# Kernel optimization log

Hardware: AMD Instinct MI355X
Metric: run time of the kernel (lower is better)

The kernel has to match this reference:

```python
import jax, jax.numpy as jnp
import numpy as np

B, T, D, C = 8, 4096, 768, 2048

def setup_inputs() -> dict:
    key = jax.random.key(0)
    k1, k2 = jax.random.split(key)
    embed = jax.random.normal(k1, (B, T, D), dtype=jnp.float32)
    cluster_centers = jax.random.normal(k2, (C, D), dtype=jnp.float32)
    return {"embed": embed, "cluster_centers": cluster_centers}

def reference(embed, cluster_centers):
    x_sq = jnp.sum(embed * embed, axis=-1, keepdims=True)          # (b, t, 1)
    c_sq = jnp.sum(cluster_centers * cluster_centers, axis=-1)     # (c,)
    cross = jnp.einsum('btd,cd->btc', embed, cluster_centers)      # (b, t, c)
    sq_dists = x_sq + c_sq[None, None, :] - 2.0 * cross
    dists = jnp.sqrt(jnp.maximum(sq_dists, 0.0))
    # dists argmax of -cdist == argmin of cdist
    clusters = jnp.argmin(dists, axis=-1)                          # (b, t) int
    return clusters
```

## Files before the change

kernel.cpp:

```cpp
#include <hip/hip_runtime.h>

typedef __fp16 f16x2 __attribute__((ext_vector_type(2)));
typedef __fp16 f16x8 __attribute__((ext_vector_type(8)));
typedef float f32x4 __attribute__((ext_vector_type(4)));

constexpr int MM = 32768;
constexpr int NN = 2048;
constexpr int KK = 768;
constexpr int NKT = KK / 32;
constexpr int NA_UNITS = (MM / 16) * NKT;
constexpr int NB_UNITS = (NN / 16) * NKT;

constexpr size_t WS_APACK = 0;
constexpr size_t WS_BPACK = WS_APACK + (size_t)MM * KK * 4;
constexpr size_t WS_CSQ   = WS_BPACK + (size_t)NN * KK * 4;
constexpr size_t WS_SLOT  = WS_CSQ + (size_t)NN * 4;
constexpr size_t WS_NEED  = WS_SLOT + (size_t)MM * 16 * 8;

__device__ __forceinline__ unsigned bc(f16x2 h) {
    return __builtin_bit_cast(unsigned, h);
}


__global__ __launch_bounds__(256)
void fragpack_kernel(const float* __restrict__ A, const float* __restrict__ Bc,
                     uint4* __restrict__ Ap, uint4* __restrict__ Bp,
                     float* __restrict__ csq) {
    const int task = blockIdx.x * 4 + (threadIdx.x >> 6);
    const int lane = threadIdx.x & 63;

    if (task >= NA_UNITS + NB_UNITS) {
        const int cl = task - (NA_UNITS + NB_UNITS);
        const float4* row = reinterpret_cast<const float4*>(Bc + (size_t)cl * KK);
        float s = 0.f;
#pragma unroll
        for (int w = 0; w < KK / (4 * 64); ++w) {
            float4 v = row[w * 64 + lane];
            s = fmaf(v.x, v.x, s); s = fmaf(v.y, v.y, s);
            s = fmaf(v.z, v.z, s); s = fmaf(v.w, v.w, s);
        }
#pragma unroll
        for (int off = 32; off > 0; off >>= 1) s += __shfl_xor(s, off, 64);
        if (lane == 0) csq[cl] = s;
        return;
    }

    const int ln15 = lane & 15;
    const int quad = lane >> 4;

    const bool isB = task >= NA_UNITS;
    const int t = isB ? task - NA_UNITS : task;
    const int tile = t / NKT, kt = t % NKT;
    const float* src = (isB ? Bc : A) + (size_t)(tile * 16 + ln15) * KK + kt * 32 + quad * 8;
    uint4* dst = (isB ? Bp : Ap) + (size_t)t * 128 + lane;

    const float4 v0 = *(const float4*)(src);
    const float4 v1 = *(const float4*)(src + 4);
    f16x2 h0 = __builtin_amdgcn_cvt_pkrtz(v0.x, v0.y);
    f16x2 h1 = __builtin_amdgcn_cvt_pkrtz(v0.z, v0.w);
    f16x2 h2 = __builtin_amdgcn_cvt_pkrtz(v1.x, v1.y);
    f16x2 h3 = __builtin_amdgcn_cvt_pkrtz(v1.z, v1.w);
    f16x2 l0 = __builtin_amdgcn_cvt_pkrtz(v0.x-(float)h0[0], v0.y-(float)h0[1]);
    f16x2 l1 = __builtin_amdgcn_cvt_pkrtz(v0.z-(float)h1[0], v0.w-(float)h1[1]);
    f16x2 l2 = __builtin_amdgcn_cvt_pkrtz(v1.x-(float)h2[0], v1.y-(float)h2[1]);
    f16x2 l3 = __builtin_amdgcn_cvt_pkrtz(v1.z-(float)h3[0], v1.w-(float)h3[1]);
    uint4 hv = {bc(h0), bc(h1), bc(h2), bc(h3)};
    uint4 lv = {bc(l0), bc(l1), bc(l2), bc(l3)};
    dst[0]  = hv;
    dst[64] = lv;
}

__global__ __launch_bounds__(64)
void csq_kernel(const float* __restrict__ cc, float* __restrict__ csq) {
    const int cl = blockIdx.x;
    const int lane = threadIdx.x;
    const float4* row = reinterpret_cast<const float4*>(cc + (size_t)cl * KK);
    float s = 0.f;
#pragma unroll
    for (int w = 0; w < KK / (4 * 64); ++w) {
        float4 v = row[w * 64 + lane];
        s = fmaf(v.x, v.x, s); s = fmaf(v.y, v.y, s);
        s = fmaf(v.z, v.z, s); s = fmaf(v.w, v.w, s);
    }
#pragma unroll
    for (int off = 32; off > 0; off >>= 1) s += __shfl_xor(s, off, 64);
    if (lane == 0) csq[cl] = s;
}

#define MF2(a, b, c) __builtin_amdgcn_mfma_f32_16x16x32_f16(a, b, c, 0, 0, 0)
#define DSB() __builtin_amdgcn_sched_barrier(0)

__global__ __launch_bounds__(256, 2)
void gemm_pack_kernel(const uint4* __restrict__ Ap, const uint4* __restrict__ Bp,
                      const float* __restrict__ csq, uint2* __restrict__ slots) {
    __shared__ uint4 ldsq[4096];

    const int b   = blockIdx.x;
    const int xcd = b & 7;
    const int s   = b >> 3;
    const int gx  = s & 15;
    const int gy  = xcd + ((s >> 4) << 3);

    const int tid  = threadIdx.x;
    const int lane = tid & 63;
    const int ln15 = lane & 15;
    const int quad = lane >> 4;
    const int wave = tid >> 6;
    const int wm   = wave >> 1;
    const int wn   = wave & 1;
    const int tbase = gy * 128;
    const int cb    = gx * 128;

    const uint4* sp[8];
#pragma unroll
    for (int q = 0; q < 8; ++q) {
        const int u = wave * 8 + q;
        const bool isA = u < 16;
        const int v = isA ? u : u - 16;
        const int tile = (isA ? gy * 8 : gx * 8) + (v >> 1);
        const int part = v & 1;
        sp[q] = (isA ? Ap : Bp) + (size_t)tile * NKT * 128 + part * 64 + lane;
    }

#define STAGE2(kt_, bufq_, q_) {                                              \
    _Pragma("unroll")                                                         \
    for (int qq = (q_); qq < (q_) + 2; ++qq)                                  \
        __builtin_amdgcn_global_load_lds(                                     \
            (const __attribute__((address_space(1))) unsigned int*)(sp[qq] + (kt_) * 128), \
            (__attribute__((address_space(3))) unsigned int*)&ldsq[(bufq_) + (wave * 8 + qq) * 64], \
            16, 0, 0); }

    f32x4 acc[4][4];
#pragma unroll
    for (int i = 0; i < 4; ++i)
#pragma unroll
        for (int j = 0; j < 4; ++j) { f32x4 z = {0.f,0.f,0.f,0.f}; acc[i][j] = z; }

    f16x8 Bh[4], Bl[4];
    f16x8 Ah[2], Al[2];

#define RD_B(bufq_) {                                                         \
    _Pragma("unroll")                                                         \
    for (int j = 0; j < 4; ++j) {                                             \
        const int nu = 16 + (wn * 4 + j) * 2;                                 \
        Bh[j] = *(const f16x8*)&ldsq[(bufq_) + nu * 64 + lane];               \
        Bl[j] = *(const f16x8*)&ldsq[(bufq_) + (nu + 1) * 64 + lane];         \
    } }

#define RD_A(bufq_, i_, s_) {                                                 \
    const int au = (wm * 4 + (i_)) * 2;                                       \
    Ah[s_] = *(const f16x8*)&ldsq[(bufq_) + au * 64 + lane];                  \
    Al[s_] = *(const f16x8*)&ldsq[(bufq_) + (au + 1) * 64 + lane]; }

#define MFMA_I(i_, s_) {                                                      \
    __builtin_amdgcn_s_setprio(1);                                            \
    _Pragma("unroll")                                                         \
    for (int j = 0; j < 4; ++j) acc[i_][j] = MF2(Ah[s_], Bh[j], acc[i_][j]);  \
    _Pragma("unroll")                                                         \
    for (int j = 0; j < 4; ++j) acc[i_][j] = MF2(Ah[s_], Bl[j], acc[i_][j]);  \
    _Pragma("unroll")                                                         \
    for (int j = 0; j < 4; ++j) acc[i_][j] = MF2(Al[s_], Bh[j], acc[i_][j]);  \
    __builtin_amdgcn_s_setprio(0); }

    STAGE2(0, 0, 0) STAGE2(0, 0, 2) STAGE2(0, 0, 4) STAGE2(0, 0, 6)

#pragma unroll 1
    for (int kt = 0; kt < NKT; ++kt) {
        const int bufq = (kt & 1) ? 2048 : 0;
        const int nxt  = bufq ^ 2048;
        const bool sn  = (kt + 1 < NKT);

        if (sn) {
            STAGE2(kt + 1, nxt, 0)
            asm volatile("s_waitcnt vmcnt(2)" ::: "memory");
        } else {
            asm volatile("s_waitcnt vmcnt(0)" ::: "memory");
        }
        DSB(); __builtin_amdgcn_s_barrier(); DSB();

        RD_B(bufq)
        RD_A(bufq, 0, 0)
        DSB();
        RD_A(bufq, 1, 1)
        if (sn) STAGE2(kt + 1, nxt, 2)
        DSB();
        MFMA_I(0, 0)
        DSB();
        RD_A(bufq, 2, 0)
        if (sn) STAGE2(kt + 1, nxt, 4)
        DSB();
        MFMA_I(1, 1)
        DSB();
        RD_A(bufq, 3, 1)
        if (sn) STAGE2(kt + 1, nxt, 6)
        DSB();
        MFMA_I(2, 0)
        DSB();
        MFMA_I(3, 1)
        DSB(); __builtin_amdgcn_s_barrier(); DSB();
    }

    float csq4[4];
#pragma unroll
    for (int j = 0; j < 4; ++j) csq4[j] = csq[cb + wn * 64 + j * 16 + ln15];

    float bval[16]; int bidx[16];
#pragma unroll
    for (int i = 0; i < 4; ++i)
#pragma unroll
        for (int r = 0; r < 4; ++r) {
            const int rid = i * 4 + r;
            float bv_ = csq4[0] - 2.0f * acc[i][0][r];
            int   bi_ = cb + wn * 64 + ln15;
#pragma unroll
            for (int j = 1; j < 4; ++j) {
                const float s2 = csq4[j] - 2.0f * acc[i][j][r];
                const int   c = cb + wn * 64 + j * 16 + ln15;
                if (s2 < bv_) { bv_ = s2; bi_ = c; }
            }
            bval[rid] = bv_; bidx[rid] = bi_;
        }
#pragma unroll
    for (int off = 1; off < 16; off <<= 1) {
#pragma unroll
        for (int rid = 0; rid < 16; ++rid) {
            const float ov = __shfl_xor(bval[rid], off, 64);
            const int   oi = __shfl_xor(bidx[rid], off, 64);
            if (ov < bval[rid] || (ov == bval[rid] && oi < bidx[rid])) {
                bval[rid] = ov; bidx[rid] = oi;
            }
        }
    }

    __syncthreads();
    float* vtab = (float*)&ldsq[0];
    int*   itab = (int*)&ldsq[64];
    if (ln15 == 0) {
#pragma unroll
        for (int i = 0; i < 4; ++i)
#pragma unroll
            for (int r = 0; r < 4; ++r) {
                const int row = wm * 64 + i * 16 + quad * 4 + r;
                vtab[row * 2 + wn] = bval[i * 4 + r];
                itab[row * 2 + wn] = bidx[i * 4 + r];
            }
    }
    __syncthreads();
    if (tid < 128) {
        float v0 = vtab[tid * 2]; int i0 = itab[tid * 2];
        const float v1 = vtab[tid * 2 + 1]; const int i1 = itab[tid * 2 + 1];
        if (v1 < v0 || (v1 == v0 && i1 < i0)) { v0 = v1; i0 = i1; }
        uint2 e; e.x = __float_as_uint(v0); e.y = (unsigned)i0;
        slots[(size_t)(tbase + tid) * 16 + gx] = e;
    }
}

__global__ __launch_bounds__(256)
void slot_reduce_kernel(const uint2* __restrict__ slots, int* __restrict__ out) {
    const int t = blockIdx.x * 256 + threadIdx.x;
    const uint2* s = slots + (size_t)t * 16;
    float bv = __uint_as_float(s[0].x); int bi = (int)s[0].y;
#pragma unroll
    for (int j = 1; j < 16; ++j) {
        const uint2 e = s[j];
        const float v = __uint_as_float(e.x);
        if (v < bv || (v == bv && (int)e.y < bi)) { bv = v; bi = (int)e.y; }
    }
    out[t] = bi;
}


__global__ __launch_bounds__(256)
void init_ws_kernel(unsigned long long* __restrict__ w) {
    w[blockIdx.x * 256 + threadIdx.x] = 0xFFFFFFFFFFFFFFFFull;
}

__global__ __launch_bounds__(256, 2)
void argmin_mfma_kernel(const float* __restrict__ A, const float* __restrict__ Bc,
                        const float* __restrict__ csq,
                        unsigned long long* __restrict__ ws64) {
    __shared__ unsigned lds[4 * 128 * 20];
    constexpr int AH = 0, AL = 2560, BH = 5120;

    const int tid  = threadIdx.x;
    const int lane = tid & 63;
    const int ln15 = lane & 15;
    const int quad = lane >> 4;
    const int wave = tid >> 6;
    const int wm = wave >> 1, wn = wave & 1;
    const int tbase = blockIdx.x * 128;
    const int cb    = blockIdx.y * 128;

    const int sr  = tid >> 1;
    const int skh = tid & 1;
    const float* gA = A  + (size_t)(tbase + sr) * KK + skh * 16;
    const float* gB = Bc + (size_t)(cb   + sr) * KK + skh * 16;
    const int wword = sr * 20 + skh * 8;

    f32x4 acc[4][4];
#pragma unroll
    for (int i = 0; i < 4; ++i)
#pragma unroll
        for (int j = 0; j < 4; ++j) { f32x4 z = {0.f,0.f,0.f,0.f}; acc[i][j] = z; }

    float4 av[4], bv[4];
#pragma unroll
    for (int p = 0; p < 4; ++p) {
        av[p] = *(const float4*)(gA + p * 4);
        bv[p] = *(const float4*)(gB + p * 4);
    }

    int aw[4], bw[4];
#pragma unroll
    for (int i = 0; i < 4; ++i) {
        aw[i] = AH + (wm * 64 + i * 16 + ln15) * 20 + quad * 4;
        bw[i] = BH + (wn * 64 + i * 16 + ln15) * 20 + quad * 4;
    }

    for (int k0 = 0; k0 < KK; k0 += 32) {
        __syncthreads();
#pragma unroll
        for (int h = 0; h < 2; ++h) {
            float4 v0 = av[2*h], v1 = av[2*h+1];
            f16x2 h00 = __builtin_amdgcn_cvt_pkrtz(v0.x, v0.y);
            f16x2 h01 = __builtin_amdgcn_cvt_pkrtz(v0.z, v0.w);
            f16x2 h10 = __builtin_amdgcn_cvt_pkrtz(v1.x, v1.y);
            f16x2 h11 = __builtin_amdgcn_cvt_pkrtz(v1.z, v1.w);
            f16x2 l00 = __builtin_amdgcn_cvt_pkrtz(v0.x-(float)h00[0], v0.y-(float)h00[1]);
            f16x2 l01 = __builtin_amdgcn_cvt_pkrtz(v0.z-(float)h01[0], v0.w-(float)h01[1]);
            f16x2 l10 = __builtin_amdgcn_cvt_pkrtz(v1.x-(float)h10[0], v1.y-(float)h10[1]);
            f16x2 l11 = __builtin_amdgcn_cvt_pkrtz(v1.z-(float)h11[0], v1.w-(float)h11[1]);
            uint4 hv = {bc(h00), bc(h01), bc(h10), bc(h11)};
            uint4 lv = {bc(l00), bc(l01), bc(l10), bc(l11)};
            *(uint4*)&lds[AH + wword + 4*h] = hv;
            *(uint4*)&lds[AL + wword + 4*h] = lv;

            float4 w0 = bv[2*h], w1 = bv[2*h+1];
            f16x2 g00 = __builtin_amdgcn_cvt_pkrtz(w0.x, w0.y);
            f16x2 g01 = __builtin_amdgcn_cvt_pkrtz(w0.z, w0.w);
            f16x2 g10 = __builtin_amdgcn_cvt_pkrtz(w1.x, w1.y);
            f16x2 g11 = __builtin_amdgcn_cvt_pkrtz(w1.z, w1.w);
            f16x2 m00 = __builtin_amdgcn_cvt_pkrtz(w0.x-(float)g00[0], w0.y-(float)g00[1]);
            f16x2 m01 = __builtin_amdgcn_cvt_pkrtz(w0.z-(float)g01[0], w0.w-(float)g01[1]);
            f16x2 m10 = __builtin_amdgcn_cvt_pkrtz(w1.x-(float)g10[0], w1.y-(float)g10[1]);
            f16x2 m11 = __builtin_amdgcn_cvt_pkrtz(w1.z-(float)g11[0], w1.w-(float)g11[1]);
            uint4 gv = {bc(g00), bc(g01), bc(g10), bc(g11)};
            uint4 mv = {bc(m00), bc(m01), bc(m10), bc(m11)};
            *(uint4*)&lds[BH + wword + 4*h]        = gv;
            *(uint4*)&lds[BH + 2560 + wword + 4*h] = mv;
        }
        __syncthreads();

        const int kn = k0 + 32;
        if (kn < KK) {
#pragma unroll
            for (int p = 0; p < 4; ++p) {
                av[p] = *(const float4*)(gA + kn + p * 4);
                bv[p] = *(const float4*)(gB + kn + p * 4);
            }
        }

        f16x8 a_h[4], a_l[4], b_h[4], b_l[4];
#pragma unroll
        for (int i = 0; i < 4; ++i) {
            a_h[i] = *(const f16x8*)&lds[aw[i]];
            a_l[i] = *(const f16x8*)&lds[aw[i] + 2560];
            b_h[i] = *(const f16x8*)&lds[bw[i]];
            b_l[i] = *(const f16x8*)&lds[bw[i] + 2560];
        }
#pragma unroll
        for (int i = 0; i < 4; ++i)
#pragma unroll
            for (int j = 0; j < 4; ++j) {
                acc[i][j] = __builtin_amdgcn_mfma_f32_16x16x32_f16(a_h[i], b_h[j], acc[i][j], 0, 0, 0);
                acc[i][j] = __builtin_amdgcn_mfma_f32_16x16x32_f16(a_h[i], b_l[j], acc[i][j], 0, 0, 0);
                acc[i][j] = __builtin_amdgcn_mfma_f32_16x16x32_f16(a_l[i], b_h[j], acc[i][j], 0, 0, 0);
            }
    }

    float csq4[4];
#pragma unroll
    for (int j = 0; j < 4; ++j) csq4[j] = csq[cb + wn * 64 + j * 16 + ln15];

    float bval[16]; int bidx[16];
#pragma unroll
    for (int i = 0; i < 4; ++i)
#pragma unroll
        for (int r = 0; r < 4; ++r) {
            const int rid = i * 4 + r;
            float bv_ = csq4[0] - 2.0f * acc[i][0][r];
            int   bi_ = cb + wn * 64 + ln15;
#pragma unroll
            for (int j = 1; j < 4; ++j) {
                const float s = csq4[j] - 2.0f * acc[i][j][r];
                const int   c = cb + wn * 64 + j * 16 + ln15;
                if (s < bv_) { bv_ = s; bi_ = c; }
            }
            bval[rid] = bv_; bidx[rid] = bi_;
        }
#pragma unroll
    for (int off = 1; off < 16; off <<= 1) {
#pragma unroll
        for (int rid = 0; rid < 16; ++rid) {
            const float ov = __shfl_xor(bval[rid], off, 64);
            const int   oi = __shfl_xor(bidx[rid], off, 64);
            if (ov < bval[rid] || (ov == bval[rid] && oi < bidx[rid])) {
                bval[rid] = ov; bidx[rid] = oi;
            }
        }
    }

    __syncthreads();
    float* vtab = (float*)&lds[0];
    int*   itab = (int*)&lds[256];
    if (ln15 == 0) {
#pragma unroll
        for (int i = 0; i < 4; ++i)
#pragma unroll
            for (int r = 0; r < 4; ++r) {
                const int row = wm * 64 + i * 16 + quad * 4 + r;
                vtab[row * 2 + wn] = bval[i * 4 + r];
                itab[row * 2 + wn] = bidx[i * 4 + r];
            }
    }
    __syncthreads();
    if (tid < 128) {
        float v0 = vtab[tid * 2]; int i0 = itab[tid * 2];
        const float v1 = vtab[tid * 2 + 1]; const int i1 = itab[tid * 2 + 1];
        if (v1 < v0 || (v1 == v0 && i1 < i0)) { v0 = v1; i0 = i1; }
        const unsigned b   = __float_as_uint(v0);
        const unsigned key = (b & 0x80000000u) ? ~b : (b | 0x80000000u);
        const unsigned long long pk =
            ((unsigned long long)key << 32) | (unsigned long long)(unsigned)i0;
        atomicMin(&ws64[tbase + tid], pk);
    }
}

__global__ __launch_bounds__(256)
void unpack_kernel(const unsigned long long* __restrict__ w, int* __restrict__ out) {
    const int i = blockIdx.x * 256 + threadIdx.x;
    out[i] = (int)(unsigned)(w[i] & 0xFFFFFFFFull);
}

extern "C" void kernel_launch(void* const* d_in, const int* in_sizes, int n_in,
                              void* d_out, int out_size, void* d_ws, size_t ws_size,
                              hipStream_t stream) {
    const float* embed   = (const float*)d_in[0];
    const float* centers = (const float*)d_in[1];
    int* out = (int*)d_out;

    if (ws_size >= WS_NEED) {
        uint4* Ap = (uint4*)((char*)d_ws + WS_APACK);
        uint4* Bp = (uint4*)((char*)d_ws + WS_BPACK);
        float* csq   = (float*)((char*)d_ws + WS_CSQ);
        uint2* slots = (uint2*)((char*)d_ws + WS_SLOT);
        fragpack_kernel<<<(NA_UNITS + NB_UNITS + NN) / 4, 256, 0, stream>>>(
            embed, centers, Ap, Bp, csq);
        gemm_pack_kernel<<<(MM / 128) * (NN / 128), 256, 0, stream>>>(
            Ap, Bp, csq, slots);
        slot_reduce_kernel<<<MM / 256, 256, 0, stream>>>(slots, out);
    } else {
        unsigned long long* ws64 = (unsigned long long*)d_ws;
        float* csq = (float*)((char*)d_ws + (size_t)MM * 8);
        init_ws_kernel<<<MM / 256, 256, 0, stream>>>(ws64);
        csq_kernel<<<NN, 64, 0, stream>>>(centers, csq);
        argmin_mfma_kernel<<<dim3(MM / 128, NN / 128), 256, 0, stream>>>(
            embed, centers, csq, ws64);
        unpack_kernel<<<MM / 256, 256, 0, stream>>>(ws64, out);
    }
}
```

Measured before the change: 425.6 us.

## Double-buffer GEMM fragments in registers with ping-pong LDS staging

Rewrites the K loop to process two k-tiles per iteration. All A/B fragments for the next tile are preloaded from LDS into a second register set while MFMAs run on the current set. Each k-tile is now staged into LDS with one batch of eight global_load_lds calls instead of four interleaved pairs, and the s_setprio hints are dropped. The goal is to hide LDS read latency behind matrix math, at the cost of roughly doubling fragment VGPR use, which may lower occupancy or cause spills.

```diff
diff --git a/kernel.cpp b/kernel.cpp
--- a/kernel.cpp
+++ b/kernel.cpp
@@ -122,82 +122,81 @@
         sp[q] = (isA ? Ap : Bp) + (size_t)tile * NKT * 128 + part * 64 + lane;
     }
 
-#define STAGE2(kt_, bufq_, q_) {                                              \
-    _Pragma("unroll")                                                         \
-    for (int qq = (q_); qq < (q_) + 2; ++qq)                                  \
+#define STAGE_ALL(kt_, bufq_) { if ((kt_) < NKT) {                            \
+    _Pragma("unroll")                                                         \
+    for (int qq = 0; qq < 8; ++qq)                                            \
         __builtin_amdgcn_global_load_lds(                                     \
             (const __attribute__((address_space(1))) unsigned int*)(sp[qq] + (kt_) * 128), \
             (__attribute__((address_space(3))) unsigned int*)&ldsq[(bufq_) + (wave * 8 + qq) * 64], \
-            16, 0, 0); }
-
-    f32x4 acc[4][4];
-#pragma unroll
-    for (int i = 0; i < 4; ++i)
-#pragma unroll
-        for (int j = 0; j < 4; ++j) { f32x4 z = {0.f,0.f,0.f,0.f}; acc[i][j] = z; }
-
-    f16x8 Bh[4], Bl[4];
-    f16x8 Ah[2], Al[2];
-
-#define RD_B(bufq_) {                                                         \
+            16, 0, 0); } }
+
+#define RD_SET(Ah_, Al_, Bh_, Bl_, bufq_) {                                   \
     _Pragma("unroll")                                                         \
     for (int j = 0; j < 4; ++j) {                                             \
         const int nu = 16 + (wn * 4 + j) * 2;                                 \
-        Bh[j] = *(const f16x8*)&ldsq[(bufq_) + nu * 64 + lane];               \
-        Bl[j] = *(const f16x8*)&ldsq[(bufq_) + (nu + 1) * 64 + lane];         \
+        Bh_[j] = *(const f16x8*)&ldsq[(bufq_) + nu * 64 + lane];              \
+        Bl_[j] = *(const f16x8*)&ldsq[(bufq_) + (nu + 1) * 64 + lane];        \
+    }                                                                         \
+    _Pragma("unroll")                                                         \
+    for (int i = 0; i < 4; ++i) {                                             \
+        const int au = (wm * 4 + i) * 2;                                      \
+        Ah_[i] = *(const f16x8*)&ldsq[(bufq_) + au * 64 + lane];              \
+        Al_[i] = *(const f16x8*)&ldsq[(bufq_) + (au + 1) * 64 + lane];        \
     } }
 
-#define RD_A(bufq_, i_, s_) {                                                 \
-    const int au = (wm * 4 + (i_)) * 2;                                       \
-    Ah[s_] = *(const f16x8*)&ldsq[(bufq_) + au * 64 + lane];                  \
-    Al[s_] = *(const f16x8*)&ldsq[(bufq_) + (au + 1) * 64 + lane]; }
-
-#define MFMA_I(i_, s_) {                                                      \
-    __builtin_amdgcn_s_setprio(1);                                            \
-    _Pragma("unroll")                                                         \
-    for (int j = 0; j < 4; ++j) acc[i_][j] = MF2(Ah[s_], Bh[j], acc[i_][j]);  \
-    _Pragma("unroll")                                                         \
-    for (int j = 0; j < 4; ++j) acc[i_][j] = MF2(Ah[s_], Bl[j], acc[i_][j]);  \
-    _Pragma("unroll")                                                         \
-    for (int j = 0; j < 4; ++j) acc[i_][j] = MF2(Al[s_], Bh[j], acc[i_][j]);  \
-    __builtin_amdgcn_s_setprio(0); }
-
-    STAGE2(0, 0, 0) STAGE2(0, 0, 2) STAGE2(0, 0, 4) STAGE2(0, 0, 6)
+#define MFMA_I2(Ah_, Al_, Bh_, Bl_, i_) {                                     \
+    _Pragma("unroll")                                                         \
+    for (int j = 0; j < 4; ++j) acc[i_][j] = MF2(Ah_[i_], Bh_[j], acc[i_][j]);\
+    _Pragma("unroll")                                                         \
+    for (int j = 0; j < 4; ++j) acc[i_][j] = MF2(Ah_[i_], Bl_[j], acc[i_][j]);\
+    _Pragma("unroll")                                                         \
+    for (int j = 0; j < 4; ++j) acc[i_][j] = MF2(Al_[i_], Bh_[j], acc[i_][j]);\
+}
+
+#define WAIT_VM0()   { asm volatile("s_waitcnt vmcnt(0)" ::: "memory"); DSB(); }
+#define WAIT_LGKM0() { asm volatile("s_waitcnt lgkmcnt(0)" ::: "memory"); DSB(); }
+#define BARRIER()    { DSB(); __builtin_amdgcn_s_barrier(); DSB(); }
+
+    f32x4 acc[4][4];
+#pragma unroll
+    for (int i = 0; i < 4; ++i)
+#pragma unroll
+        for (int j = 0; j < 4; ++j) { f32x4 z = {0.f,0.f,0.f,0.f}; acc[i][j] = z; }
+
+    f16x8 Ah0[4], Al0[4], Bh0[4], Bl0[4];
+    f16x8 Ah1[4], Al1[4], Bh1[4], Bl1[4];
+
+    STAGE_ALL(0, 0)
+    WAIT_VM0(); BARRIER();
+    RD_SET(Ah0, Al0, Bh0, Bl0, 0)
+    STAGE_ALL(1, 2048)
+    WAIT_LGKM0();
 
 #pragma unroll 1
-    for (int kt = 0; kt < NKT; ++kt) {
-        const int bufq = (kt & 1) ? 2048 : 0;
-        const int nxt  = bufq ^ 2048;
-        const bool sn  = (kt + 1 < NKT);
-
-        if (sn) {
-            STAGE2(kt + 1, nxt, 0)
-            asm volatile("s_waitcnt vmcnt(2)" ::: "memory");
-        } else {
-            asm volatile("s_waitcnt vmcnt(0)" ::: "memory");
-        }
-        DSB(); __builtin_amdgcn_s_barrier(); DSB();
-
-        RD_B(bufq)
-        RD_A(bufq, 0, 0)
-        DSB();
-        RD_A(bufq, 1, 1)
-        if (sn) STAGE2(kt + 1, nxt, 2)
-        DSB();
-        MFMA_I(0, 0)
-        DSB();
-        RD_A(bufq, 2, 0)
-        if (sn) STAGE2(kt + 1, nxt, 4)
-        DSB();
-        MFMA_I(1, 1)
-        DSB();
-        RD_A(bufq, 3, 1)
-        if (sn) STAGE2(kt + 1, nxt, 6)
-        DSB();
-        MFMA_I(2, 0)
-        DSB();
-        MFMA_I(3, 1)
-        DSB(); __builtin_amdgcn_s_barrier(); DSB();
+    for (int kt = 0; kt < NKT; kt += 2) {
+        MFMA_I2(Ah0, Al0, Bh0, Bl0, 0)
+        MFMA_I2(Ah0, Al0, Bh0, Bl0, 1)
+        DSB();
+        WAIT_VM0(); BARRIER();
+        RD_SET(Ah1, Al1, Bh1, Bl1, 2048)
+        STAGE_ALL(kt + 2, 0)
+        DSB();
+        MFMA_I2(Ah0, Al0, Bh0, Bl0, 2)
+        MFMA_I2(Ah0, Al0, Bh0, Bl0, 3)
+        DSB();
+        WAIT_LGKM0();
+
+        MFMA_I2(Ah1, Al1, Bh1, Bl1, 0)
+        MFMA_I2(Ah1, Al1, Bh1, Bl1, 1)
+        DSB();
+        WAIT_VM0(); BARRIER();
+        if (kt + 2 < NKT) { RD_SET(Ah0, Al0, Bh0, Bl0, 0) }
+        STAGE_ALL(kt + 3, 2048)
+        DSB();
+        MFMA_I2(Ah1, Al1, Bh1, Bl1, 2)
+        MFMA_I2(Ah1, Al1, Bh1, Bl1, 3)
+        DSB();
+        WAIT_LGKM0();
     }
 
     float csq4[4];
```

Result: slower. 456.1 us (+7.2%).
